# Kernel optimization log

Hardware: AMD Instinct MI355X
Metric: run time of the kernel (lower is better)

The kernel has to match this reference:

```python
import jax, jax.numpy as jnp
import numpy as np
import math

B, S, DM, L = 4, 512, 768, 2
DI, DS, K = 2 * DM, 16, 4          # mamba_ssm defaults: expand=2, d_state=16, d_conv=4
DTR = math.ceil(DM / 16)           # dt_rank = 48
F = 1


def setup_inputs() -> dict:
    key = jax.random.key(0)
    ks = iter(jax.random.split(key, 16))
    g = lambda shape, s=0.02: jax.random.normal(next(ks), shape, jnp.float32) * s
    # sinusoidal positional encoding (precomputed buffer)
    pos = np.arange(S)[:, None].astype(np.float32)
    div = np.exp(np.arange(0, DM, 2).astype(np.float32) * (-math.log(10000.0) / DM))
    pe = np.zeros((S, DM), np.float32)
    pe[:, 0::2] = np.sin(pos * div)
    pe[:, 1::2] = np.cos(pos * div)
    # S4D-real style A init
    A_log = jnp.broadcast_to(jnp.log(jnp.arange(1, DS + 1, dtype=jnp.float32)), (L, DI, DS))
    return dict(
        x=jax.random.normal(next(ks), (B, S, F), jnp.float32),
        w_in=g((DM, F)), b_in=jnp.zeros((DM,), jnp.float32),
        pe=jnp.asarray(pe)[None],                       # (1, S, DM)
        ln1_w=jnp.ones((L, DM)), ln1_b=jnp.zeros((L, DM)),
        w_inproj=g((L, 2 * DI, DM)),
        conv_w=g((L, DI, K), 0.1), conv_b=jnp.zeros((L, DI)),
        w_xproj=g((L, DTR + 2 * DS, DI)),
        w_dt=g((L, DI, DTR)), b_dt=jnp.full((L, DI), -4.0, jnp.float32),
        A_log=A_log, D=jnp.ones((L, DI)),
        w_outproj=g((L, DM, DI)),
        ln2_w=jnp.ones((L, DM)), ln2_b=jnp.zeros((L, DM)),
        ff_w1=g((L, 2 * DM, DM)), ff_b1=jnp.zeros((L, 2 * DM)),
        ff_w2=g((L, DM, 2 * DM)), ff_b2=jnp.zeros((L, DM)),
        lnf_w=jnp.ones((DM,)), lnf_b=jnp.zeros((DM,)),
        w_head=g((1, DM)), b_head=jnp.zeros((1,), jnp.float32),
    )


def _ln(x, w, b):
    mu = x.mean(-1, keepdims=True)
    v = ((x - mu) ** 2).mean(-1, keepdims=True)
    return (x - mu) * jax.lax.rsqrt(v + 1e-5) * w + b


def _mamba(x, w_inproj, conv_w, conv_b, w_xproj, w_dt, b_dt, A_log, D_, w_outproj):
    # x: (B, S, DM)
    Bsz = x.shape[0]
    xz = jnp.einsum('bsd,ed->bse', x, w_inproj)         # (B, S, 2*DI)
    xm, z = jnp.split(xz, 2, axis=-1)
    # causal depthwise conv1d over time
    xc = jax.lax.conv_general_dilated(
        xm.transpose(0, 2, 1), conv_w[:, None, :], (1,), [(K - 1, 0)],
        feature_group_count=DI, dimension_numbers=('NCH', 'OIH', 'NCH'))
    xc = jax.nn.silu((xc + conv_b[:, None]).transpose(0, 2, 1))  # (B, S, DI)
    dbc = jnp.einsum('bsd,ed->bse', xc, w_xproj)        # (B, S, DTR+2*DS)
    dt, Bm, Cm = dbc[..., :DTR], dbc[..., DTR:DTR + DS], dbc[..., DTR + DS:]
    delta = jax.nn.softplus(jnp.einsum('bsr,dr->bsd', dt, w_dt) + b_dt)  # (B, S, DI)
    A = -jnp.exp(A_log)                                 # (DI, DS)

    def step(h, inp):
        d_t, B_t, C_t, u_t = inp                        # (B,DI),(B,DS),(B,DS),(B,DI)
        h = h * jnp.exp(d_t[:, :, None] * A) + (d_t * u_t)[:, :, None] * B_t[:, None, :]
        return h, jnp.einsum('bds,bs->bd', h, C_t)

    h0 = jnp.zeros((Bsz, DI, DS), x.dtype)
    _, ys = jax.lax.scan(step, h0, (delta.transpose(1, 0, 2), Bm.transpose(1, 0, 2),
                                    Cm.transpose(1, 0, 2), xc.transpose(1, 0, 2)))
    y = ys.transpose(1, 0, 2) + xc * D_
    y = y * jax.nn.silu(z)
    return jnp.einsum('bsd,ed->bse', y, w_outproj)


def reference(x, w_in, b_in, pe, ln1_w, ln1_b, w_inproj, conv_w, conv_b, w_xproj,
              w_dt, b_dt, A_log, D, w_outproj, ln2_w, ln2_b, ff_w1, ff_b1,
              ff_w2, ff_b2, lnf_w, lnf_b, w_head, b_head):
    h = jnp.einsum('bsf,df->bsd', x, w_in) + b_in
    h = h + pe[:, :h.shape[1]]
    for l in range(L):  # fixed small layer count
        h = h + _mamba(_ln(h, ln1_w[l], ln1_b[l]), w_inproj[l], conv_w[l], conv_b[l],
                       w_xproj[l], w_dt[l], b_dt[l], A_log[l], D[l], w_outproj[l])
        f = _ln(h, ln2_w[l], ln2_b[l])
        f = jax.nn.gelu(jnp.einsum('bsd,ed->bse', f, ff_w1[l]) + ff_b1[l], approximate=False)
        h = h + jnp.einsum('bse,de->bsd', f, ff_w2[l]) + ff_b2[l]
    h = _ln(h, lnf_w, lnf_b)
    h = h.mean(axis=1)                                  # mean pool over time
    return jnp.einsum('bd,od->bo', h, w_head) + b_head
```

## Files before the change

### kernel.cpp

```cpp
#include <hip/hip_runtime.h>
#include <hip/hip_bf16.h>
#include <math.h>

#define B_ 4
#define S_ 512
#define DM_ 768
#define L_ 2
#define DI_ 1536
#define DS_ 16
#define KC_ 4
#define DTR_ 48
#define NSEG 64
#define TS 8
#define PMN_IP ((size_t)2048 * 2 * DI_)

typedef __hip_bfloat16 bf16;
typedef __attribute__((ext_vector_type(8))) short short8;
typedef __attribute__((ext_vector_type(4))) float f32x4;

#define GLDS16(g, l) __builtin_amdgcn_global_load_lds( \
    (const __attribute__((address_space(1))) void*)(g), \
    (__attribute__((address_space(3))) void*)(l), 16, 0, 0)

typedef struct { unsigned short x, y, z, w; } us4;
__device__ __forceinline__ void cast4(const float* __restrict__ s, bf16* __restrict__ d) {
  float4 v = *(const float4*)s;
  us4 o;
  o.x = __bfloat16_as_ushort(__float2bfloat16(v.x));
  o.y = __bfloat16_as_ushort(__float2bfloat16(v.y));
  o.z = __bfloat16_as_ushort(__float2bfloat16(v.z));
  o.w = __bfloat16_as_ushort(__float2bfloat16(v.w));
  *(us4*)d = o;
}
__device__ __forceinline__ void store4z(bf16* __restrict__ d) {
  us4 o; o.x = o.y = o.z = o.w = 0;
  *(us4*)d = o;
}

__global__ __launch_bounds__(256)
void k_init(const float* __restrict__ x, const float* __restrict__ w_in,
            const float* __restrict__ b_in, const float* __restrict__ pe,
            const float* __restrict__ lw, const float* __restrict__ lb,
            float* __restrict__ h, bf16* __restrict__ xout,
            const float* __restrict__ w_inproj, const float* __restrict__ w_outproj,
            const float* __restrict__ ff_w1, const float* __restrict__ ff_w2,
            const float* __restrict__ w_xproj, const float* __restrict__ w_dt,
            const float* __restrict__ A_log,
            bf16* __restrict__ wip, bf16* __restrict__ wop,
            bf16* __restrict__ wf1, bf16* __restrict__ wf2,
            bf16* __restrict__ wxp, bf16* __restrict__ wdtp,
            float* __restrict__ At, float* __restrict__ part) {
  if (blockIdx.x < 2048) {
    __shared__ float red1[4], red2[4];
    __shared__ float s_mu, s_rstd;
    int row = blockIdx.x;
    int s = row % S_;
    float xv = x[row];
    float v[3];
    float s1 = 0.f, s2 = 0.f;
#pragma unroll
    for (int j = 0; j < 3; ++j) {
      int d = threadIdx.x + j * 256;
      float t = xv * w_in[d] + b_in[d] + pe[s * DM_ + d];
      v[j] = t;
      s1 += t; s2 += t * t;
    }
    for (int off = 32; off; off >>= 1) { s1 += __shfl_down(s1, off); s2 += __shfl_down(s2, off); }
    if ((threadIdx.x & 63) == 0) { red1[threadIdx.x >> 6] = s1; red2[threadIdx.x >> 6] = s2; }
    __syncthreads();
    if (threadIdx.x == 0) {
      float t1 = red1[0] + red1[1] + red1[2] + red1[3];
      float t2 = red2[0] + red2[1] + red2[2] + red2[3];
      float mu = t1 * (1.f / DM_);
      float var = t2 * (1.f / DM_) - mu * mu;
      s_mu = mu;
      s_rstd = rsqrtf(var + 1e-5f);
    }
    __syncthreads();
    float mu = s_mu, rstd = s_rstd;
#pragma unroll
    for (int j = 0; j < 3; ++j) {
      int d = threadIdx.x + j * 256;
      h[(size_t)row * DM_ + d] = v[j];
      xout[(size_t)row * DM_ + d] = __float2bfloat16((v[j] - mu) * rstd * lw[d] + lb[d]);
    }
    return;
  }
  if (blockIdx.x == 2048 && threadIdx.x < B_) part[threadIdx.x] = 0.f;
  const int N0 = L_ * 2 * DI_ * DM_;
  const int N1 = L_ * DM_ * DI_;
  const int N2 = L_ * 2 * DM_ * DM_;
  const int N3 = L_ * DM_ * 2 * DM_;
  const int N4 = L_ * 128 * DI_;
  const int N5 = L_ * DI_ * 64;
  const int N6 = L_ * 16 * DI_;
  const int T4 = (N0 + N1 + N2 + N3 + N4 + N5) >> 2;
  int tid = (blockIdx.x - 2048) * 256 + threadIdx.x;
  int stride = 1024 * 256;
  for (int v = tid; v < T4; v += stride) {
    int j = v << 2;
    if (j < N0) { cast4(w_inproj + j, wip + j); continue; }
    j -= N0;
    if (j < N1) { cast4(w_outproj + j, wop + j); continue; }
    j -= N1;
    if (j < N2) { cast4(ff_w1 + j, wf1 + j); continue; }
    j -= N2;
    if (j < N3) { cast4(ff_w2 + j, wf2 + j); continue; }
    j -= N3;
    if (j < N4) {
      int col = j % DI_;
      int row = (j / DI_) & 127;
      int l = j / (128 * DI_);
      if (row < 80) cast4(&w_xproj[((size_t)l * 80 + row) * DI_ + col], wxp + j);
      else store4z(wxp + j);
      continue;
    }
    j -= N4;
    {
      int col = j & 63;
      int r = (j >> 6) % DI_;
      int l = j / (DI_ * 64);
      if (col < 48) cast4(&w_dt[((size_t)l * DI_ + r) * 48 + col], wdtp + j);
      else store4z(wdtp + j);
    }
  }
  for (int j = tid; j < N6; j += stride) {
    int d = j % DI_;
    int n = (j / DI_) & 15;
    int l = j / (16 * DI_);
    At[j] = -__expf(A_log[((size_t)l * DI_ + d) * 16 + n]) * 1.4426950408889634f;
  }
}

__global__ __launch_bounds__(256)
void k_lnred(const bf16* __restrict__ pxp, int KS,
             const float* __restrict__ hin, const float* __restrict__ bias,
             const float* __restrict__ lw, const float* __restrict__ lb,
             float* __restrict__ hout, bf16* __restrict__ xout,
             const float* __restrict__ wh, float* __restrict__ headp) {
  __shared__ float red1[4], red2[4];
  __shared__ float s_mu, s_rstd;
  int row = blockIdx.x;
  float v[3];
  float s1 = 0.f, s2 = 0.f;
#pragma unroll
  for (int j = 0; j < 3; ++j) {
    int n = threadIdx.x + j * 256;
    float s = hin[(size_t)row * DM_ + n];
    if (bias) s += bias[n];
    for (int ks = 0; ks < KS; ++ks)
      s += __bfloat162float(pxp[(size_t)ks * 2048 * DM_ + (size_t)row * DM_ + n]);
    v[j] = s;
    s1 += s; s2 += s * s;
  }
  for (int off = 32; off; off >>= 1) { s1 += __shfl_down(s1, off); s2 += __shfl_down(s2, off); }
  if ((threadIdx.x & 63) == 0) { red1[threadIdx.x >> 6] = s1; red2[threadIdx.x >> 6] = s2; }
  __syncthreads();
  if (threadIdx.x == 0) {
    float t1 = red1[0] + red1[1] + red1[2] + red1[3];
    float t2 = red2[0] + red2[1] + red2[2] + red2[3];
    float mu = t1 * (1.f / DM_);
    float var = t2 * (1.f / DM_) - mu * mu;
    s_mu = mu;
    s_rstd = rsqrtf(var + 1e-5f);
  }
  __syncthreads();
  float mu = s_mu, rstd = s_rstd;
  float hacc = 0.f;
#pragma unroll
  for (int j = 0; j < 3; ++j) {
    int n = threadIdx.x + j * 256;
    float vl = (v[j] - mu) * rstd * lw[n] + lb[n];
    hout[(size_t)row * DM_ + n] = v[j];
    xout[(size_t)row * DM_ + n] = __float2bfloat16(vl);
    if (headp) hacc += vl * wh[n];
  }
  if (headp) {
    __syncthreads();
    for (int off = 32; off; off >>= 1) hacc += __shfl_down(hacc, off);
    if ((threadIdx.x & 63) == 0) red1[threadIdx.x >> 6] = hacc;
    __syncthreads();
    if (threadIdx.x == 0)
      atomicAdd(headp + row / S_, red1[0] + red1[1] + red1[2] + red1[3]);
  }
}

__global__ void k_gelred(const bf16* __restrict__ pxp, const float* __restrict__ bias,
                         bf16* __restrict__ out) {
  int idx = blockIdx.x * 256 + threadIdx.x;
  if (idx >= 2048 * 2 * DM_) return;
  int n = idx % (2 * DM_);
  float s = __bfloat162float(pxp[idx]) +
            __bfloat162float(pxp[(size_t)2048 * 2 * DM_ + idx]) + bias[n];
  s = 0.5f * s * (1.f + erff(s * 0.70710678118654752f));
  out[idx] = __float2bfloat16(s);
}

__global__ void k_conv_silu(const bf16* __restrict__ pip, const float* __restrict__ cw,
                            const float* __restrict__ cb, bf16* __restrict__ xcb) {
  int idx = blockIdx.x * 256 + threadIdx.x;
  if (idx >= B_ * S_ * (DI_ / 2)) return;
  int d2 = idx % (DI_ / 2);
  int d = d2 * 2;
  int t = idx / (DI_ / 2);
  int s = t % S_;
  int b = t / S_;
  float a0 = cb[d], a1 = cb[d + 1];
  const bf16* p0 = pip + (size_t)(b * S_) * (2 * DI_) + d;
  const bf16* p1 = p0 + PMN_IP;
#pragma unroll
  for (int k = 0; k < KC_; ++k) {
    int ss = s - (KC_ - 1) + k;
    if (ss >= 0) {
      ushort2 u0 = *(const ushort2*)&p0[(size_t)ss * (2 * DI_)];
      ushort2 u1 = *(const ushort2*)&p1[(size_t)ss * (2 * DI_)];
      float x0 = __bfloat162float(__ushort_as_bfloat16(u0.x)) +
                 __bfloat162float(__ushort_as_bfloat16(u1.x));
      float x1 = __bfloat162float(__ushort_as_bfloat16(u0.y)) +
                 __bfloat162float(__ushort_as_bfloat16(u1.y));
      a0 = fmaf(x0, cw[d * KC_ + k], a0);
      a1 = fmaf(x1, cw[(d + 1) * KC_ + k], a1);
    }
  }
  float v0 = a0 / (1.f + expf(-a0));
  float v1 = a1 / (1.f + expf(-a1));
  ushort2 o;
  o.x = __bfloat16_as_ushort(__float2bfloat16(v0));
  o.y = __bfloat16_as_ushort(__float2bfloat16(v1));
  *(ushort2*)&xcb[(size_t)t * DI_ + d] = o;
}

__global__ __launch_bounds__(256)
void k_scanA(const bf16* __restrict__ dtp, const bf16* __restrict__ wdt_l,
             const float* __restrict__ bdt_l,
             const bf16* __restrict__ xcb, const float* __restrict__ bc,
             const float* __restrict__ At, const float* __restrict__ Dv,
             float* __restrict__ ylocal, float* __restrict__ cumd,
             float* __restrict__ hend) {
  int b = blockIdx.y;
  int seg = blockIdx.z;
  int d = blockIdx.x * 256 + threadIdx.x;
  int s0 = seg * TS;

  float A[16], hst[16];
#pragma unroll
  for (int n = 0; n < 16; ++n) {
    A[n] = At[(size_t)n * DI_ + d];
    hst[n] = 0.f;
  }
  float wdt[48];
  {
    const bf16* wrow = wdt_l + (size_t)d * 64;
#pragma unroll
    for (int k = 0; k < 48; ++k) wdt[k] = __bfloat162float(wrow[k]);
  }
  float bdt = bdt_l[d];
  float Dd = Dv[d];
  float cd = 0.f;

  const unsigned int* dru = (const unsigned int*)(dtp) + (size_t)(b * S_ + s0) * 32;
  const bf16* up = xcb + ((size_t)(b * S_ + s0)) * DI_ + d;
  const float* bp = bc + ((size_t)(b * S_ + s0)) * 32;
  float* yp = ylocal + ((size_t)(b * S_ + s0)) * DI_ + d;
  float* cp = cumd + ((size_t)(b * S_ + s0)) * DI_ + d;

  float u_next = __bfloat162float(up[0]);
#pragma unroll
  for (int s = 0; s < TS; ++s) {
    float u = u_next;
    if (s + 1 < TS) u_next = __bfloat162float(up[(size_t)(s + 1) * DI_]);
    float acc = bdt;
#pragma unroll
    for (int kk = 0; kk < 24; ++kk) {
      unsigned int w2 = dru[s * 32 + kk];
      acc = fmaf(__uint_as_float(w2 << 16), wdt[2 * kk], acc);
      acc = fmaf(__uint_as_float(w2 & 0xffff0000u), wdt[2 * kk + 1], acc);
    }
    float dl = (acc > 20.f) ? acc : log1pf(__expf(acc));
    cd += dl;
    float dlu = dl * u;
    float y = 0.f;
#pragma unroll
    for (int n = 0; n < 16; ++n) {
      float e = exp2f(dl * A[n]);
      hst[n] = fmaf(hst[n], e, dlu * bp[s * 32 + n]);
      y = fmaf(hst[n], bp[s * 32 + 16 + n], y);
    }
    yp[(size_t)s * DI_] = fmaf(u, Dd, y);
    cp[(size_t)s * DI_] = cd;
  }
  float* hp = hend + ((size_t)(b * NSEG + seg) * 16) * DI_ + d;
#pragma unroll
  for (int n = 0; n < 16; ++n) hp[(size_t)n * DI_] = hst[n];
}

__global__ void k_scanB(const float* __restrict__ hend, const float* __restrict__ cumd,
                        const float* __restrict__ At, float* __restrict__ h0seg) {
  int idx = blockIdx.x * 256 + threadIdx.x;
  if (idx >= B_ * 16 * DI_) return;
  int d = idx % DI_;
  int r = idx / DI_;
  int n = r & 15;
  int b = r >> 4;
  float A = At[(size_t)n * DI_ + d];
  float h0 = 0.f;
  for (int seg = 0; seg < NSEG; ++seg) {
    size_t o = ((size_t)(b * NSEG + seg) * 16 + n) * DI_ + d;
    h0seg[o] = h0;
    float cdt = cumd[((size_t)(b * S_ + seg * TS + TS - 1)) * DI_ + d];
    h0 = h0 * exp2f(A * cdt) + hend[o];
  }
}

__global__ __launch_bounds__(256)
void k_scanC(const float* __restrict__ ylocal, const float* __restrict__ cumd,
             const float* __restrict__ bc, const float* __restrict__ At,
             const float* __restrict__ h0seg, const bf16* __restrict__ pip,
             bf16* __restrict__ yb16) {
  int d = blockIdx.x * 256 + threadIdx.x;
  int t = blockIdx.y;
  int b = blockIdx.z;
  int seg = t / TS;
  size_t o = ((size_t)(b * S_ + t)) * DI_ + d;
  float y = ylocal[o];
  if (seg) {
    float cd = cumd[o];
    const float* Cp = bc + ((size_t)(b * S_ + t)) * 32 + 16;
    const float* Hb = h0seg + ((size_t)(b * NSEG + seg) * 16) * DI_ + d;
#pragma unroll
    for (int n = 0; n < 16; ++n)
      y += Cp[n] * exp2f(At[(size_t)n * DI_ + d] * cd) * Hb[(size_t)n * DI_];
  }
  size_t oz = ((size_t)(b * S_ + t)) * (2 * DI_) + DI_ + d;
  float z = __bfloat162float(pip[oz]) + __bfloat162float(pip[PMN_IP + oz]);
  float sig = 1.f / (1.f + __expf(-z));
  yb16[o] = __float2bfloat16(y * (z * sig));
}

__global__ void k_head2(const float* __restrict__ part, const float* __restrict__ bh,
                        float* __restrict__ out) {
  int b = threadIdx.x;
  if (b < B_) out[b] = part[b] * (1.f / S_) + bh[0];
}

template <int EPI>
__global__ __launch_bounds__(256)
void k_gemm_mfma(const bf16* __restrict__ A, int lda,
                 const bf16* __restrict__ W, int ldw,
                 const float* __restrict__ bias,
                 void* __restrict__ out1,
                 int ldc, int N, int Kdim, int pmn) {
  __shared__ short As[2][8192];
  __shared__ short Bs[2][8192];

  int nwg = gridDim.x * gridDim.y;
  int orig = blockIdx.y * gridDim.x + blockIdx.x;
  int wg = (nwg % 8 == 0) ? ((orig & 7) * (nwg >> 3) + (orig >> 3)) : orig;
  int m0 = (wg / gridDim.x) * 128;
  int n0 = (wg % gridDim.x) * 128;

  int lane = threadIdx.x & 63;
  int wid = threadIdx.x >> 6;
  int wm = wid >> 1, wn = wid & 1;
  int lr = lane & 15;
  int ch = lane >> 4;
  int koff = blockIdx.z * Kdim;

  f32x4 acc[4][4];
#pragma unroll
  for (int i = 0; i < 4; ++i)
#pragma unroll
    for (int j = 0; j < 4; ++j) {
      acc[i][j][0] = 0.f; acc[i][j][1] = 0.f; acc[i][j][2] = 0.f; acc[i][j][3] = 0.f;
    }

#define GSTAGE(bb, kt)                                                            \
  {                                                                               \
    int k0 = koff + (kt) * 64;                                                    \
    _Pragma("unroll")                                                             \
    for (int c0 = 0; c0 < 4; ++c0) {                                              \
      int c = c0 * 256 + (int)threadIdx.x;                                        \
      int row = c & 127, chk = c >> 7;                                            \
      GLDS16(A + (size_t)(m0 + row) * lda + k0 + chk * 8,                         \
             (char*)&As[bb][0] + c * 16);                                         \
      GLDS16(W + (size_t)(n0 + row) * ldw + k0 + chk * 8,                         \
             (char*)&Bs[bb][0] + c * 16);                                         \
    }                                                                             \
  }

  int nt = Kdim / 64;
  GSTAGE(0, 0);

  for (int t = 0; t < nt; ++t) {
    int buf = t & 1;
    if (t + 1 < nt) {
      GSTAGE(buf ^ 1, t + 1);
      asm volatile("s_waitcnt vmcnt(8)" ::: "memory");
    } else {
      asm volatile("s_waitcnt vmcnt(0)" ::: "memory");
    }
    __builtin_amdgcn_s_barrier();
    __builtin_amdgcn_sched_barrier(0);

    short8 a0[4], a1[4], b0[4], b1[4];
#pragma unroll
    for (int f = 0; f < 4; ++f) {
      a0[f] = *(const short8*)&As[buf][(ch * 128 + wm * 64 + f * 16 + lr) * 8];
      b0[f] = *(const short8*)&Bs[buf][(ch * 128 + wn * 64 + f * 16 + lr) * 8];
    }
    __builtin_amdgcn_sched_barrier(0);
#pragma unroll
    for (int f = 0; f < 4; ++f) {
      a1[f] = *(const short8*)&As[buf][((4 + ch) * 128 + wm * 64 + f * 16 + lr) * 8];
      b1[f] = *(const short8*)&Bs[buf][((4 + ch) * 128 + wn * 64 + f * 16 + lr) * 8];
    }
    asm volatile("s_waitcnt lgkmcnt(8)" ::: "memory");
    __builtin_amdgcn_sched_barrier(0);
    __builtin_amdgcn_s_setprio(1);
#pragma unroll
    for (int i = 0; i < 4; ++i)
#pragma unroll
      for (int j = 0; j < 4; ++j)
        acc[i][j] = __builtin_amdgcn_mfma_f32_16x16x32_bf16(a0[i], b0[j], acc[i][j], 0, 0, 0);
    __builtin_amdgcn_sched_barrier(0);
    asm volatile("s_waitcnt lgkmcnt(0)" ::: "memory");
    __builtin_amdgcn_sched_barrier(0);
#pragma unroll
    for (int i = 0; i < 4; ++i)
#pragma unroll
      for (int j = 0; j < 4; ++j)
        acc[i][j] = __builtin_amdgcn_mfma_f32_16x16x32_bf16(a1[i], b1[j], acc[i][j], 0, 0, 0);
    __builtin_amdgcn_s_setprio(0);
    __builtin_amdgcn_sched_barrier(0);
    __builtin_amdgcn_s_barrier();
  }
#undef GSTAGE

#pragma unroll
  for (int i = 0; i < 4; ++i) {
#pragma unroll
    for (int j = 0; j < 4; ++j) {
      int nl = wn * 64 + j * 16 + (lane & 15);
      int n = n0 + nl;
#pragma unroll
      for (int q = 0; q < 4; ++q) {
        int m = m0 + wm * 64 + i * 16 + (lane >> 4) * 4 + q;
        float v = acc[i][j][q];
        if (EPI == 0) {
          ((float*)out1)[(size_t)m * ldc + n] = v;
        } else if (EPI == 3) {
          v += bias[n];
          v = (v > 20.f) ? v : log1pf(expf(v));
          ((float*)out1)[(size_t)m * ldc + n] = v;
        } else if (EPI == 5) {
          ((float*)out1)[(size_t)blockIdx.z * pmn + (size_t)m * N + n] = v;
        } else if (EPI == 6) {
          ((bf16*)out1)[(size_t)m * ldc + n] = __float2bfloat16(v);
        } else if (EPI == 7) {
          ((bf16*)out1)[(size_t)blockIdx.z * pmn + (size_t)m * N + n] = __float2bfloat16(v);
        }
      }
    }
  }
}

__global__ void k_xreduce(const float* __restrict__ pxp, bf16* __restrict__ dtp,
                          float* __restrict__ bcb) {
  int idx = blockIdx.x * 256 + threadIdx.x;
  if (idx >= 2048 * 128) return;
  int m = idx >> 7, n = idx & 127;
  float s = 0.f;
#pragma unroll
  for (int k = 0; k < 8; ++k) s += pxp[(size_t)k * 2048 * 128 + idx];
  if (n < 64) dtp[m * 64 + n] = __float2bfloat16(n < 48 ? s : 0.f);
  if (n >= 48 && n < 80) bcb[m * 32 + (n - 48)] = s;
}


extern "C" void kernel_launch(void* const* d_in, const int* in_sizes, int n_in,
                              void* d_out, int out_size, void* d_ws, size_t ws_size,
                              hipStream_t stream) {
  const float* x        = (const float*)d_in[0];
  const float* w_in     = (const float*)d_in[1];
  const float* b_in     = (const float*)d_in[2];
  const float* pe       = (const float*)d_in[3];
  const float* ln1_w    = (const float*)d_in[4];
  const float* ln1_b    = (const float*)d_in[5];
  const float* w_inproj = (const float*)d_in[6];
  const float* conv_w   = (const float*)d_in[7];
  const float* conv_b   = (const float*)d_in[8];
  const float* w_xproj  = (const float*)d_in[9];
  const float* w_dt     = (const float*)d_in[10];
  const float* b_dt     = (const float*)d_in[11];
  const float* A_log    = (const float*)d_in[12];
  const float* Dv       = (const float*)d_in[13];
  const float* w_outproj= (const float*)d_in[14];
  const float* ln2_w    = (const float*)d_in[15];
  const float* ln2_b    = (const float*)d_in[16];
  const float* ff_w1    = (const float*)d_in[17];
  const float* ff_b1    = (const float*)d_in[18];
  const float* ff_w2    = (const float*)d_in[19];
  const float* ff_b2    = (const float*)d_in[20];
  const float* lnf_w    = (const float*)d_in[21];
  const float* lnf_b    = (const float*)d_in[22];
  const float* w_head   = (const float*)d_in[23];
  const float* b_head   = (const float*)d_in[24];
  float* out = (float*)d_out;

  const int M = B_ * S_;

  float* wsf = (float*)d_ws;
  float* h    = wsf; wsf += (size_t)M * DM_;
  float* bc   = wsf; wsf += (size_t)M * 32;
  float* ylocal = wsf; wsf += (size_t)M * DI_;
  float* cumd = wsf; wsf += (size_t)M * DI_;
  float* hend = wsf; wsf += (size_t)B_ * NSEG * DI_ * 16;
  float* h0sg = wsf; wsf += (size_t)B_ * NSEG * DI_ * 16;
  float* pxp  = wsf; wsf += (size_t)4 * M * 2 * DM_;
  float* At   = wsf; wsf += (size_t)L_ * 16 * DI_;
  float* part = wsf; wsf += 64;
  bf16* wsb = (bf16*)wsf;
  bf16* xln16 = wsb; wsb += (size_t)M * DM_;
  bf16* pip   = wsb; wsb += 2 * PMN_IP;
  bf16* xcb   = wsb; wsb += (size_t)M * DI_;
  bf16* dtp   = wsb; wsb += (size_t)M * 64;
  bf16* yb16  = wsb; wsb += (size_t)M * DI_;
  bf16* ffh16 = wsb; wsb += (size_t)M * DI_;
  bf16* wip   = wsb; wsb += (size_t)L_ * 2 * DI_ * DM_;
  bf16* wxp   = wsb; wsb += (size_t)L_ * 128 * DI_;
  bf16* wdtp  = wsb; wsb += (size_t)L_ * DI_ * 64;
  bf16* wop   = wsb; wsb += (size_t)L_ * DM_ * DI_;
  bf16* wf1   = wsb; wsb += (size_t)L_ * 2 * DM_ * DM_;
  bf16* wf2   = wsb; wsb += (size_t)L_ * DM_ * 2 * DM_;

  bf16* pxp16 = (bf16*)pxp;

  dim3 blk(256);

  k_init<<<2048 + 1024, blk, 0, stream>>>(
      x, w_in, b_in, pe, ln1_w, ln1_b, h, xln16,
      w_inproj, w_outproj, ff_w1, ff_w2, w_xproj, w_dt, A_log,
      wip, wop, wf1, wf2, wxp, wdtp, At, part);

  for (int l = 0; l < L_; ++l) {
    const float* Atl = At + (size_t)l * 16 * DI_;

    k_gemm_mfma<7><<<dim3(2 * DI_ / 128, M / 128, 2), blk, 0, stream>>>(
        xln16, DM_, wip + (size_t)l * 2 * DI_ * DM_, DM_, nullptr,
        pip, 2 * DI_, 2 * DI_, DM_ / 2, (int)PMN_IP);

    k_conv_silu<<<(B_ * S_ * (DI_ / 2) + 255) / 256, blk, 0, stream>>>(
        pip, conv_w + l * DI_ * KC_, conv_b + l * DI_, xcb);

    k_gemm_mfma<5><<<dim3(1, M / 128, 8), blk, 0, stream>>>(
        xcb, DI_, wxp + (size_t)l * 128 * DI_, DI_, nullptr,
        pxp, 128, 128, DI_ / 8, M * 128);
    k_xreduce<<<(M * 128) / 256, blk, 0, stream>>>(pxp, dtp, bc);

    k_scanA<<<dim3(DI_ / 256, B_, NSEG), blk, 0, stream>>>(
        dtp, wdtp + (size_t)l * DI_ * 64, b_dt + l * DI_,
        xcb, bc, Atl, Dv + l * DI_, ylocal, cumd, hend);
    k_scanB<<<(B_ * 16 * DI_ + 255) / 256, blk, 0, stream>>>(hend, cumd, Atl, h0sg);
    k_scanC<<<dim3(DI_ / 256, S_, B_), blk, 0, stream>>>(
        ylocal, cumd, bc, Atl, h0sg, pip, yb16);

    k_gemm_mfma<7><<<dim3(DM_ / 128, M / 128, 4), blk, 0, stream>>>(
        yb16, DI_, wop + (size_t)l * DM_ * DI_, DI_, nullptr,
        pxp16, DM_, DM_, DI_ / 4, M * DM_);
    k_lnred<<<M, blk, 0, stream>>>(pxp16, 4, h, nullptr,
                                   ln2_w + l * DM_, ln2_b + l * DM_, h, xln16,
                                   nullptr, nullptr);

    k_gemm_mfma<7><<<dim3(2 * DM_ / 128, M / 128, 2), blk, 0, stream>>>(
        xln16, DM_, wf1 + (size_t)l * 2 * DM_ * DM_, DM_, nullptr,
        pxp16, 2 * DM_, 2 * DM_, DM_ / 2, M * 2 * DM_);
    k_gelred<<<(M * 2 * DM_) / 256, blk, 0, stream>>>(pxp16, ff_b1 + l * 2 * DM_, ffh16);

    k_gemm_mfma<7><<<dim3(DM_ / 128, M / 128, 4), blk, 0, stream>>>(
        ffh16, 2 * DM_, wf2 + (size_t)l * DM_ * 2 * DM_, 2 * DM_, nullptr,
        pxp16, DM_, DM_, DI_ / 4, M * DM_);
    const float* nlw = (l + 1 < L_) ? ln1_w + (l + 1) * DM_ : lnf_w;
    const float* nlb = (l + 1 < L_) ? ln1_b + (l + 1) * DM_ : lnf_b;
    const float* whp = (l + 1 < L_) ? nullptr : w_head;
    float* hpp = (l + 1 < L_) ? nullptr : part;
    k_lnred<<<M, blk, 0, stream>>>(pxp16, 4, h, ff_b2 + l * DM_, nlw, nlb, h, xln16,
                                   whp, hpp);
  }

  k_head2<<<1, 64, 0, stream>>>(part, b_head, out);
}
```

Measured before the change: 509.7 us.

## Halve scan segments, transpose packed dt weights for coalesced loads

```diff
diff --git a/kernel.cpp b/kernel.cpp
--- a/kernel.cpp
+++ b/kernel.cpp
@@ -10,8 +10,8 @@
 #define DS_ 16
 #define KC_ 4
 #define DTR_ 48
-#define NSEG 64
-#define TS 8
+#define NSEG 32
+#define TS 16
 #define PMN_IP ((size_t)2048 * 2 * DI_)
 
 typedef __hip_bfloat16 bf16;
@@ -48,7 +48,7 @@
             const float* __restrict__ A_log,
             bf16* __restrict__ wip, bf16* __restrict__ wop,
             bf16* __restrict__ wf1, bf16* __restrict__ wf2,
-            bf16* __restrict__ wxp, bf16* __restrict__ wdtp,
+            bf16* __restrict__ wxp, unsigned int* __restrict__ wdtu,
             float* __restrict__ At, float* __restrict__ part) {
   if (blockIdx.x < 2048) {
     __shared__ float red1[4], red2[4];
@@ -92,9 +92,9 @@
   const int N2 = L_ * 2 * DM_ * DM_;
   const int N3 = L_ * DM_ * 2 * DM_;
   const int N4 = L_ * 128 * DI_;
-  const int N5 = L_ * DI_ * 64;
   const int N6 = L_ * 16 * DI_;
-  const int T4 = (N0 + N1 + N2 + N3 + N4 + N5) >> 2;
+  const int NU = L_ * 24 * DI_;
+  const int T4 = (N0 + N1 + N2 + N3 + N4) >> 2;
   int tid = (blockIdx.x - 2048) * 256 + threadIdx.x;
   int stride = 1024 * 256;
   for (int v = tid; v < T4; v += stride) {
@@ -107,22 +107,22 @@
     j -= N2;
     if (j < N3) { cast4(ff_w2 + j, wf2 + j); continue; }
     j -= N3;
-    if (j < N4) {
+    {
       int col = j % DI_;
       int row = (j / DI_) & 127;
       int l = j / (128 * DI_);
       if (row < 80) cast4(&w_xproj[((size_t)l * 80 + row) * DI_ + col], wxp + j);
       else store4z(wxp + j);
-      continue;
-    }
-    j -= N4;
-    {
-      int col = j & 63;
-      int r = (j >> 6) % DI_;
-      int l = j / (DI_ * 64);
-      if (col < 48) cast4(&w_dt[((size_t)l * DI_ + r) * 48 + col], wdtp + j);
-      else store4z(wdtp + j);
-    }
+    }
+  }
+  for (int j = tid; j < NU; j += stride) {
+    int d = j % DI_;
+    int k2 = (j / DI_) % 24;
+    int l = j / (24 * DI_);
+    const float* wr = w_dt + ((size_t)l * DI_ + d) * 48 + 2 * k2;
+    unsigned int lo = __bfloat16_as_ushort(__float2bfloat16(wr[0]));
+    unsigned int hi = __bfloat16_as_ushort(__float2bfloat16(wr[1]));
+    wdtu[j] = lo | (hi << 16);
   }
   for (int j = tid; j < N6; j += stride) {
     int d = j % DI_;
@@ -231,7 +231,7 @@
 }
 
 __global__ __launch_bounds__(256)
-void k_scanA(const bf16* __restrict__ dtp, const bf16* __restrict__ wdt_l,
+void k_scanA(const bf16* __restrict__ dtp, const unsigned int* __restrict__ wdtu_l,
              const float* __restrict__ bdt_l,
              const bf16* __restrict__ xcb, const float* __restrict__ bc,
              const float* __restrict__ At, const float* __restrict__ Dv,
@@ -250,9 +250,13 @@
   }
   float wdt[48];
   {
-    const bf16* wrow = wdt_l + (size_t)d * 64;
-#pragma unroll
-    for (int k = 0; k < 48; ++k) wdt[k] = __bfloat162float(wrow[k]);
+    const unsigned int* wrow = wdtu_l + d;
+#pragma unroll
+    for (int k2 = 0; k2 < 24; ++k2) {
+      unsigned int w2 = wrow[(size_t)k2 * DI_];
+      wdt[2 * k2]     = __uint_as_float(w2 << 16);
+      wdt[2 * k2 + 1] = __uint_as_float(w2 & 0xffff0000u);
+    }
   }
   float bdt = bdt_l[d];
   float Dd = Dv[d];
@@ -265,7 +269,7 @@
   float* cp = cumd + ((size_t)(b * S_ + s0)) * DI_ + d;
 
   float u_next = __bfloat162float(up[0]);
-#pragma unroll
+#pragma unroll 4
   for (int s = 0; s < TS; ++s) {
     float u = u_next;
     if (s + 1 < TS) u_next = __bfloat162float(up[(size_t)(s + 1) * DI_]);
@@ -519,6 +523,7 @@
   float* pxp  = wsf; wsf += (size_t)4 * M * 2 * DM_;
   float* At   = wsf; wsf += (size_t)L_ * 16 * DI_;
   float* part = wsf; wsf += 64;
+  unsigned int* wdtu = (unsigned int*)wsf; wsf += (size_t)L_ * 24 * DI_;
   bf16* wsb = (bf16*)wsf;
   bf16* xln16 = wsb; wsb += (size_t)M * DM_;
   bf16* pip   = wsb; wsb += 2 * PMN_IP;
@@ -528,7 +533,6 @@
   bf16* ffh16 = wsb; wsb += (size_t)M * DI_;
   bf16* wip   = wsb; wsb += (size_t)L_ * 2 * DI_ * DM_;
   bf16* wxp   = wsb; wsb += (size_t)L_ * 128 * DI_;
-  bf16* wdtp  = wsb; wsb += (size_t)L_ * DI_ * 64;
   bf16* wop   = wsb; wsb += (size_t)L_ * DM_ * DI_;
   bf16* wf1   = wsb; wsb += (size_t)L_ * 2 * DM_ * DM_;
   bf16* wf2   = wsb; wsb += (size_t)L_ * DM_ * 2 * DM_;
@@ -540,7 +544,7 @@
   k_init<<<2048 + 1024, blk, 0, stream>>>(
       x, w_in, b_in, pe, ln1_w, ln1_b, h, xln16,
       w_inproj, w_outproj, ff_w1, ff_w2, w_xproj, w_dt, A_log,
-      wip, wop, wf1, wf2, wxp, wdtp, At, part);
+      wip, wop, wf1, wf2, wxp, wdtu, At, part);
 
   for (int l = 0; l < L_; ++l) {
     const float* Atl = At + (size_t)l * 16 * DI_;
@@ -558,7 +562,7 @@
     k_xreduce<<<(M * 128) / 256, blk, 0, stream>>>(pxp, dtp, bc);
 
     k_scanA<<<dim3(DI_ / 256, B_, NSEG), blk, 0, stream>>>(
-        dtp, wdtp + (size_t)l * DI_ * 64, b_dt + l * DI_,
+        dtp, wdtu + (size_t)l * 24 * DI_, b_dt + l * DI_,
         xcb, bc, Atl, Dv + l * DI_, ylocal, cumd, hend);
     k_scanB<<<(B_ * 16 * DI_ + 255) / 256, blk, 0, stream>>>(hend, cumd, Atl, h0sg);
     k_scanC<<<dim3(DI_ / 256, S_, B_), blk, 0, stream>>>(
```

After: 497.6 us. -2.4%, faster.
